# Performance work log

Measured on AMD Instinct MI355X. Metric: run time of the kernel, lower is better.

## Reference

```python
import math
import jax, jax.numpy as jnp
import numpy as np

T_LEN, BATCH = 215, 256
D_INP = 36; D_MODEL = 36          # d_model must be 36 for internal dims to be consistent
D_T = D_MODEL + 36                # 72: transformer encoder width
N_HEAD = 4; D_HEAD = D_T // N_HEAD
D_FF = 128; N_LAYERS = 2; D_STATIC = 9; N_CLASSES = 2
N_NODES = 36

def _layer_norm(x, g, b, eps=1e-5):
    mu = jnp.mean(x, -1, keepdims=True)
    var = jnp.mean((x - mu) ** 2, -1, keepdims=True)
    return (x - mu) / jnp.sqrt(var + eps) * g + b

def _forward(src, static, times, lengths, W_enc, b_enc, W_emb, b_emb, Wq, bq, Wk, bk, Wv, bv, Wskip, bskip, enc_in_w, enc_in_b, enc_out_w, enc_out_b, enc_ff1_w, enc_ff1_b, enc_ff2_w, enc_ff2_b, enc_ln1_g, enc_ln1_b, enc_ln2_g, enc_ln2_b, mlp_w1, mlp_b1, mlp_w2, mlp_b2):
    T, B = src.shape[0], src.shape[1]
    x = (src[:, :, :D_INP] @ W_enc.T + b_enc) * math.sqrt(D_MODEL)          # [T,B,36]
    # positional encoding: 18 timescales = max_len ** linspace(0,1,18)
    timescales = jnp.asarray(215.0 ** np.linspace(0.0, 1.0, D_MODEL // 2), jnp.float32)
    scaled = times[:, :, None] / timescales                                  # [T,B,18]
    pe = jnp.concatenate([jnp.sin(scaled), jnp.cos(scaled)], -1)             # [T,B,36]
    emb = static @ W_emb.T + b_emb                                           # [B,36]
    mask = jnp.arange(T)[None, :] >= lengths[:, None]                        # [B,T] True = pad
    # --- batched TransformerConv over fully-connected 36-node graph (replaces per-sample loop) ---
    q = x @ Wq.T + bq; k = x @ Wk.T + bk; v = x @ Wv.T + bv
    skip = x @ Wskip.T + bskip
    scores = jnp.einsum('ibe,jbe->bij', q[:N_NODES], k[:N_NODES]) / math.sqrt(36.0)  # i=tgt, j=src
    A = jax.nn.softmax(scores, -1)                      # per-target softmax over incoming edges
    msg = jnp.einsum('bij,jbe->ibe', A, v[:N_NODES])    # edge_weights are all ones
    gout = skip.at[:N_NODES].add(msg)                   # [T,B,36]; rows >= 36 have no in-edges
    # per-edge alpha flattened in nonzero(adj) order: e = src*36 + tgt
    alpha_all = A.transpose(0, 2, 1).reshape(B, N_NODES * N_NODES).T         # [1296,B]
    sq = jnp.sum(alpha_all ** 2, 0)
    d2 = jnp.maximum(sq[:, None] + sq[None, :] - 2.0 * (alpha_all.T @ alpha_all), 0.0)
    distance = jnp.mean(jnp.sqrt(jnp.where(d2 > 0, d2, 1.0)) * (d2 > 0))     # mean pairwise L2
    # --- 2-layer post-norm transformer encoder, width 72, key padding mask ---
    h = jnp.concatenate([gout, pe], -1)                                      # [T,B,72]
    neg = jnp.where(mask[:, None, None, :], -1e9, 0.0)                       # [B,1,1,T]
    for l in range(N_LAYERS):
        qkv = h @ enc_in_w[l].T + enc_in_b[l]
        qh, kh, vh = [t.reshape(T, B, N_HEAD, D_HEAD) for t in jnp.split(qkv, 3, -1)]
        s = jnp.einsum('tbhd,sbhd->bhts', qh, kh) / math.sqrt(D_HEAD) + neg
        ctx = jnp.einsum('bhts,sbhd->tbhd', jax.nn.softmax(s, -1), vh).reshape(T, B, D_T)
        h = _layer_norm(h + ctx @ enc_out_w[l].T + enc_out_b[l], enc_ln1_g[l], enc_ln1_b[l])
        ff = jax.nn.relu(h @ enc_ff1_w[l].T + enc_ff1_b[l]) @ enc_ff2_w[l].T + enc_ff2_b[l]
        h = _layer_norm(h + ff, enc_ln2_g[l], enc_ln2_b[l])
    # masked mean over time, denominator lengths+1 (as in original)
    valid = (~mask).astype(h.dtype).T[:, :, None]                            # [T,B,1]
    pooled = jnp.sum(h * valid, 0) / (lengths.astype(h.dtype)[:, None] + 1.0)
    feat = jnp.concatenate([pooled, emb], -1)                                # [B,108]
    logits = jax.nn.relu(feat @ mlp_w1.T + mlp_b1) @ mlp_w2.T + mlp_b2
    return logits, distance

def setup_inputs() -> dict:
    key = jax.random.key(0)
    ks = jax.random.split(key, 40)
    def nrm(i, shape, s=0.05):
        return jax.random.normal(ks[i], shape, jnp.float32) * s
    return {
        'src': jax.random.normal(ks[0], (T_LEN, BATCH, 2 * D_INP), jnp.float32),
        'static': jax.random.normal(ks[1], (BATCH, D_STATIC), jnp.float32),
        'times': jnp.tile(jnp.arange(T_LEN, dtype=jnp.float32)[:, None], (1, BATCH)),
        'lengths': jax.random.randint(ks[2], (BATCH,), 1, T_LEN + 1),
        'W_enc': nrm(3, (D_MODEL, D_INP)), 'b_enc': jnp.zeros((D_MODEL,), jnp.float32),
        'W_emb': nrm(4, (D_MODEL, D_STATIC)), 'b_emb': jnp.zeros((D_MODEL,), jnp.float32),
        'Wq': nrm(5, (36, 36)), 'bq': nrm(6, (36,)),
        'Wk': nrm(7, (36, 36)), 'bk': nrm(8, (36,)),
        'Wv': nrm(9, (36, 36)), 'bv': nrm(10, (36,)),
        'Wskip': nrm(11, (36, 36)), 'bskip': nrm(12, (36,)),
        'enc_in_w': nrm(13, (N_LAYERS, 3 * D_T, D_T)), 'enc_in_b': nrm(14, (N_LAYERS, 3 * D_T)),
        'enc_out_w': nrm(15, (N_LAYERS, D_T, D_T)), 'enc_out_b': nrm(16, (N_LAYERS, D_T)),
        'enc_ff1_w': nrm(17, (N_LAYERS, D_FF, D_T)), 'enc_ff1_b': nrm(18, (N_LAYERS, D_FF)),
        'enc_ff2_w': nrm(19, (N_LAYERS, D_T, D_FF)), 'enc_ff2_b': nrm(20, (N_LAYERS, D_T)),
        'enc_ln1_g': jnp.ones((N_LAYERS, D_T), jnp.float32), 'enc_ln1_b': jnp.zeros((N_LAYERS, D_T), jnp.float32),
        'enc_ln2_g': jnp.ones((N_LAYERS, D_T), jnp.float32), 'enc_ln2_b': jnp.zeros((N_LAYERS, D_T), jnp.float32),
        'mlp_w1': nrm(21, (108, 108)), 'mlp_b1': nrm(22, (108,)),
        'mlp_w2': nrm(23, (N_CLASSES, 108)), 'mlp_b2': nrm(24, (N_CLASSES,)),
    }

def reference(src, static, times, lengths, W_enc, b_enc, W_emb, b_emb, Wq, bq, Wk, bk, Wv, bv, Wskip, bskip, enc_in_w, enc_in_b, enc_out_w, enc_out_b, enc_ff1_w, enc_ff1_b, enc_ff2_w, enc_ff2_b, enc_ln1_g, enc_ln1_b, enc_ln2_g, enc_ln2_b, mlp_w1, mlp_b1, mlp_w2, mlp_b2):
    return _forward(src, static, times, lengths, W_enc, b_enc, W_emb, b_emb, Wq, bq, Wk, bk, Wv, bv, Wskip, bskip, enc_in_w, enc_in_b, enc_out_w, enc_out_b, enc_ff1_w, enc_ff1_b, enc_ff2_w, enc_ff2_b, enc_ln1_g, enc_ln1_b, enc_ln2_g, enc_ln2_b, mlp_w1, mlp_b1, mlp_w2, mlp_b2)
```

## Files before the change

### kernel.cpp

```cpp
#include <hip/hip_runtime.h>

#define TT 215
#define BB 256
#define ROWS (TT * BB)

typedef __attribute__((ext_vector_type(8))) short short8;
typedef __attribute__((ext_vector_type(4))) float f32x4;

__device__ __forceinline__ unsigned short f2bf_rn(float x) {
    unsigned int u = __float_as_uint(x);
    u = u + 0x7FFFu + ((u >> 16) & 1u);
    return (unsigned short)(u >> 16);
}
__device__ __forceinline__ float bf2f(unsigned short b) {
    return __uint_as_float(((unsigned int)b) << 16);
}

__global__ void k_prep(const float* __restrict__ enc_in_w, const float* __restrict__ ff1_w,
                       const float* __restrict__ ff2_w, const float* __restrict__ enc_out_w,
                       unsigned short* __restrict__ Whi, unsigned short* __restrict__ Wlo,
                       unsigned short* __restrict__ F1hi, unsigned short* __restrict__ F1lo,
                       unsigned short* __restrict__ F2hi, unsigned short* __restrict__ F2lo,
                       unsigned short* __restrict__ Ohi, unsigned short* __restrict__ Olo,
                       float* __restrict__ ts) {
    int g = blockIdx.x * 256 + threadIdx.x;
    if (g < 18) ts[g] = (float)pow(215.0, (double)g / 17.0);
    if (g < 2 * 216 * 96) {
        int l = g / (216 * 96), rem = g % (216 * 96);
        int o = rem / 96, k = rem % 96;
        float v = (k < 72) ? enc_in_w[((size_t)l * 216 + o) * 72 + k] : 0.f;
        unsigned short hi = f2bf_rn(v);
        Whi[g] = hi; Wlo[g] = f2bf_rn(v - bf2f(hi));
    }
    if (g < 2 * 128 * 96) {
        int l = g / (128 * 96), rem = g % (128 * 96);
        int j = rem / 96, k = rem % 96;
        float v = (k < 72) ? ff1_w[((size_t)l * 128 + j) * 72 + k] : 0.f;
        unsigned short hi = f2bf_rn(v);
        F1hi[g] = hi; F1lo[g] = f2bf_rn(v - bf2f(hi));
    }
    if (g < 2 * 72 * 128) {
        float v = ff2_w[g];
        unsigned short hi = f2bf_rn(v);
        F2hi[g] = hi; F2lo[g] = f2bf_rn(v - bf2f(hi));
    }
    if (g < 2 * 72 * 96) {
        int l = g / (72 * 96), rem = g % (72 * 96);
        int o = rem / 96, k = rem % 96;
        float v = (k < 72) ? enc_out_w[((size_t)l * 72 + o) * 72 + k] : 0.f;
        unsigned short hi = f2bf_rn(v);
        Ohi[g] = hi; Olo[g] = f2bf_rn(v - bf2f(hi));
    }
}

__global__ __launch_bounds__(256, 1) void k_enc1(const float* __restrict__ src,
                                                 const float* __restrict__ W,
                                                 const float* __restrict__ bias,
                                                 float* __restrict__ x) {
    int row = blockIdx.x * 256 + threadIdx.x;
    int o0 = blockIdx.y * 9;
    float s[36];
    const float4* sv = (const float4*)(src + (size_t)row * 72);
#pragma unroll
    for (int k = 0; k < 9; ++k) {
        float4 v = sv[k];
        s[4 * k] = v.x; s[4 * k + 1] = v.y; s[4 * k + 2] = v.z; s[4 * k + 3] = v.w;
    }
    float* xp = x + (size_t)row * 36 + o0;
#pragma unroll
    for (int o = 0; o < 9; ++o) {
        float a = bias[o0 + o];
        const float* w = W + (size_t)(o0 + o) * 36;
#pragma unroll
        for (int i = 0; i < 36; ++i) a = fmaf(s[i], w[i], a);
        xp[o] = a * 6.0f;
    }
}

__global__ __launch_bounds__(256, 1) void k_enc2(const float* __restrict__ x,
                                                 const float* __restrict__ W,
                                                 const float* __restrict__ bias,
                                                 float* __restrict__ h) {
    int row = blockIdx.x * 256 + threadIdx.x;
    int o0 = blockIdx.y * 9;
    float xr[36];
    const float4* xv = (const float4*)(x + (size_t)row * 36);
#pragma unroll
    for (int k = 0; k < 9; ++k) {
        float4 v = xv[k];
        xr[4 * k] = v.x; xr[4 * k + 1] = v.y; xr[4 * k + 2] = v.z; xr[4 * k + 3] = v.w;
    }
    float* hp = h + (size_t)row * 72 + o0;
#pragma unroll
    for (int o = 0; o < 9; ++o) {
        float a = bias[o0 + o];
        const float* w = W + (size_t)(o0 + o) * 36;
#pragma unroll
        for (int i = 0; i < 36; ++i) a = fmaf(xr[i], w[i], a);
        hp[o] = a;
    }
}

__global__ __launch_bounds__(256) void k_pe(const float* __restrict__ times,
                                            const float* __restrict__ ts,
                                            float* __restrict__ h) {
    int idx = blockIdx.x * 256 + threadIdx.x;
    int d = idx % 36, row = idx / 36;
    float t = times[row];
    float val;
    if (d < 18) val = sinf(t / ts[d]);
    else        val = cosf(t / ts[d - 18]);
    h[(size_t)row * 72 + 36 + d] = val;
}

__global__ __launch_bounds__(256, 1) void k_graph_qkv(const float* __restrict__ x,
                                                      const float* __restrict__ Wq, const float* __restrict__ bq,
                                                      const float* __restrict__ Wk, const float* __restrict__ bk,
                                                      const float* __restrict__ Wv, const float* __restrict__ bv,
                                                      float* __restrict__ qg, float* __restrict__ kg,
                                                      float* __restrict__ vg) {
    int row = blockIdx.x * 256 + threadIdx.x;
    int mat = blockIdx.y >> 2;
    int o0 = (blockIdx.y & 3) * 9;
    const float* W; const float* bias; float* out;
    if (mat == 0)      { W = Wq; bias = bq; out = qg; }
    else if (mat == 1) { W = Wk; bias = bk; out = kg; }
    else               { W = Wv; bias = bv; out = vg; }
    float xr[36];
    const float4* xv = (const float4*)(x + (size_t)row * 36);
#pragma unroll
    for (int k = 0; k < 9; ++k) {
        float4 v = xv[k];
        xr[4 * k] = v.x; xr[4 * k + 1] = v.y; xr[4 * k + 2] = v.z; xr[4 * k + 3] = v.w;
    }
    float* op = out + (size_t)row * 36 + o0;
#pragma unroll
    for (int o = 0; o < 9; ++o) {
        float a = bias[o0 + o];
        const float* w = W + (size_t)(o0 + o) * 36;
#pragma unroll
        for (int i = 0; i < 36; ++i) a = fmaf(xr[i], w[i], a);
        op[o] = a;
    }
}

__global__ void k_graph_attn(const float* __restrict__ qg, const float* __restrict__ kg,
                             const float* __restrict__ vg, float* __restrict__ h,
                             unsigned short* __restrict__ Ahi, unsigned short* __restrict__ Alo,
                             float* __restrict__ sqv) {
    __shared__ float q[1296], k[1296], v[1296], A[1296];
    __shared__ float red[128];
    int b = blockIdx.x, tid = threadIdx.x;
    for (int i = tid; i < 1296; i += 128) {
        int t = i / 36, e = i % 36;
        int g = (t * BB + b) * 36 + e;
        q[i] = qg[g]; k[i] = kg[g]; v[i] = vg[g];
    }
    __syncthreads();
    for (int i = tid; i < 1296; i += 128) {
        int r = i / 36, c = i % 36;
        float a = 0.f;
#pragma unroll
        for (int e = 0; e < 36; ++e) a = fmaf(q[r * 36 + e], k[c * 36 + e], a);
        A[i] = a * (1.0f / 6.0f);
    }
    __syncthreads();
    if (tid < 36) {
        float m = -1e30f;
        for (int j = 0; j < 36; ++j) m = fmaxf(m, A[tid * 36 + j]);
        float s = 0.f;
        for (int j = 0; j < 36; ++j) { float e = expf(A[tid * 36 + j] - m); A[tid * 36 + j] = e; s += e; }
        float inv = 1.0f / s;
        for (int j = 0; j < 36; ++j) A[tid * 36 + j] *= inv;
    }
    __syncthreads();
    float lsq = 0.f;
    for (int i = tid; i < 1296; i += 128) {
        float a = A[i];
        unsigned short hi = f2bf_rn(a);
        Ahi[(size_t)b * 1312 + i] = hi;
        Alo[(size_t)b * 1312 + i] = f2bf_rn(a - bf2f(hi));
        lsq = fmaf(a, a, lsq);
        int r = i / 36, e = i % 36;
        float m = 0.f;
#pragma unroll
        for (int j = 0; j < 36; ++j) m = fmaf(A[r * 36 + j], v[j * 36 + e], m);
        h[((size_t)r * BB + b) * 72 + e] += m;
    }
    if (tid < 16) {
        Ahi[(size_t)b * 1312 + 1296 + tid] = 0;
        Alo[(size_t)b * 1312 + 1296 + tid] = 0;
    }
    red[tid] = lsq;
    __syncthreads();
    for (int s = 64; s > 0; s >>= 1) { if (tid < s) red[tid] += red[tid + s]; __syncthreads(); }
    if (tid == 0) sqv[b] = red[0];
}

__global__ __launch_bounds__(256, 1) void k_gram(const unsigned short* __restrict__ Ahi,
                                                 const unsigned short* __restrict__ Alo,
                                                 const float* __restrict__ sqv,
                                                 float* __restrict__ bpart) {
    __shared__ float red[4];
    int tid = threadIdx.x;
    int w = tid >> 6;
    int lane = tid & 63;
    int n16 = lane & 15;
    int quad = lane >> 4;
    int i0 = (blockIdx.x >> 3) * 32 + (w >> 1) * 16;
    int j0 = (blockIdx.x & 7) * 32 + (w & 1) * 16;
    const short8* Ari = (const short8*)(Ahi + (size_t)(i0 + n16) * 1312);
    const short8* Arl = (const short8*)(Alo + (size_t)(i0 + n16) * 1312);
    const short8* Bri = (const short8*)(Ahi + (size_t)(j0 + n16) * 1312);
    const short8* Brl = (const short8*)(Alo + (size_t)(j0 + n16) * 1312);
    f32x4 acc = (f32x4){0.f, 0.f, 0.f, 0.f};
    for (int k2 = 0; k2 < 41; ++k2) {
        int ko = k2 * 4 + quad;
        short8 ah = Ari[ko], al = Arl[ko];
        short8 bh = Bri[ko], bl = Brl[ko];
        acc = __builtin_amdgcn_mfma_f32_16x16x32_bf16(ah, bh, acc, 0, 0, 0);
        acc = __builtin_amdgcn_mfma_f32_16x16x32_bf16(ah, bl, acc, 0, 0, 0);
        acc = __builtin_amdgcn_mfma_f32_16x16x32_bf16(al, bh, acc, 0, 0, 0);
    }
    float part = 0.f;
#pragma unroll
    for (int reg = 0; reg < 4; ++reg) {
        int i = i0 + quad * 4 + reg;
        int j = j0 + n16;
        float d2 = fmaxf(sqv[i] + sqv[j] - 2.0f * acc[reg], 0.0f);
        part += (d2 > 0.0f) ? sqrtf(d2) : 0.0f;
    }
#pragma unroll
    for (int m = 1; m < 64; m <<= 1) part += __shfl_xor(part, m);
    if (lane == 0) red[w] = part;
    __syncthreads();
    if (tid == 0) bpart[blockIdx.x] = red[0] + red[1] + red[2] + red[3];
}

__global__ __launch_bounds__(256, 1) void k_qkv(const float* __restrict__ h,
                                                const unsigned short* __restrict__ Whi,
                                                const unsigned short* __restrict__ Wlo,
                                                const float* __restrict__ bias,
                                                float* __restrict__ qkv) {
    int tid = threadIdx.x;
    int w = tid >> 6;
    int lane = tid & 63;
    int n16 = lane & 15;
    int quad = lane >> 4;
    int m0 = blockIdx.x * 64 + w * 16;
    int r = m0 + n16;
    short8 Ahi[3], Alo[3];
#pragma unroll
    for (int s = 0; s < 3; ++s) {
        int k0 = s * 32 + quad * 8;
        float v[8];
        if (k0 < 72) {
            const float4* ap = (const float4*)(h + (size_t)r * 72 + k0);
            float4 v0 = ap[0], v1 = ap[1];
            v[0] = v0.x; v[1] = v0.y; v[2] = v0.z; v[3] = v0.w;
            v[4] = v1.x; v[5] = v1.y; v[6] = v1.z; v[7] = v1.w;
        } else {
#pragma unroll
            for (int j = 0; j < 8; ++j) v[j] = 0.f;
        }
        short8 ph, pl;
#pragma unroll
        for (int j = 0; j < 8; ++j) {
            unsigned short hi = f2bf_rn(v[j]);
            ph[j] = (short)hi;
            pl[j] = (short)f2bf_rn(v[j] - bf2f(hi));
        }
        Ahi[s] = ph; Alo[s] = pl;
    }
    f32x4 acc[14];
#pragma unroll
    for (int t = 0; t < 14; ++t) acc[t] = (f32x4){0.f, 0.f, 0.f, 0.f};
#pragma unroll
    for (int t = 0; t < 14; ++t) {
        int o = t * 16 + n16;
        int oc = (o > 215) ? 215 : o;
        const short8* bh = (const short8*)(Whi + (size_t)oc * 96);
        const short8* bl = (const short8*)(Wlo + (size_t)oc * 96);
        f32x4 a = acc[t];
#pragma unroll
        for (int s = 0; s < 3; ++s) {
            short8 Bh = bh[s * 4 + quad];
            short8 Bl = bl[s * 4 + quad];
            a = __builtin_amdgcn_mfma_f32_16x16x32_bf16(Ahi[s], Bh, a, 0, 0, 0);
            a = __builtin_amdgcn_mfma_f32_16x16x32_bf16(Ahi[s], Bl, a, 0, 0, 0);
            a = __builtin_amdgcn_mfma_f32_16x16x32_bf16(Alo[s], Bh, a, 0, 0, 0);
        }
        acc[t] = a;
    }
#pragma unroll
    for (int t = 0; t < 14; ++t) {
        int col = t * 16 + n16;
        if (col < 216) {
            float b = bias[col];
#pragma unroll
            for (int reg = 0; reg < 4; ++reg) {
                int row = m0 + quad * 4 + reg;
                qkv[(size_t)row * 216 + col] = acc[t][reg] + b;
            }
        }
    }
}

__global__ __launch_bounds__(256, 1) void k_attn(const float* __restrict__ qkv,
                                                 const int* __restrict__ lengths,
                                                 float* __restrict__ ctx) {
    __shared__ __attribute__((aligned(16))) unsigned short Kb[215 * 40];
    __shared__ __attribute__((aligned(16))) unsigned short Vt[32 * 232];
    __shared__ __attribute__((aligned(16))) unsigned short Pw[4][16 * 232];
    int b = blockIdx.x & (BB - 1);
    int hh = blockIdx.x >> 8;
    int tid = threadIdx.x;
    int len = lengths[b];
    for (int i = tid; i < (215 * 40) / 2; i += 256) ((unsigned int*)Kb)[i] = 0u;
    for (int i = tid; i < (32 * 232) / 2; i += 256) ((unsigned int*)Vt)[i] = 0u;
    __syncthreads();
    for (int i = tid; i < len * 18; i += 256) {
        int s = i / 18, d = i % 18;
        size_t base2 = ((size_t)s * BB + b) * 216 + hh * 18 + d;
        Kb[s * 40 + d] = f2bf_rn(qkv[base2 + 72]);
        Vt[d * 232 + s] = f2bf_rn(qkv[base2 + 144]);
    }
    __syncthreads();
    int w = tid >> 6;
    int lane = tid & 63;
    int n16 = lane & 15;
    int quad = lane >> 4;
    const float scale = 0.23570226039551587f;
    int nk2 = (len + 31) >> 5;
    int nkt = nk2 * 2;
    int nstrips = (len + 15) >> 4;
    unsigned short* P = &Pw[w][0];
    for (int strip = w; strip < nstrips; strip += 4) {
        int q0 = strip * 16;
        int qr = q0 + n16; if (qr > 214) qr = 214;
        float qv[8];
#pragma unroll
        for (int j = 0; j < 8; ++j) qv[j] = 0.f;
        {
            const float* qp = qkv + ((size_t)qr * BB + b) * 216 + hh * 18;
            int d0 = quad * 8;
            if (d0 < 16) {
                const float2* q2 = (const float2*)(qp + d0);
                float2 a0 = q2[0], a1 = q2[1], a2 = q2[2], a3 = q2[3];
                qv[0] = a0.x; qv[1] = a0.y; qv[2] = a1.x; qv[3] = a1.y;
                qv[4] = a2.x; qv[5] = a2.y; qv[6] = a3.x; qv[7] = a3.y;
            } else if (d0 == 16) {
                qv[0] = qp[16]; qv[1] = qp[17];
            }
        }
        short8 Qhi, Qlo;
#pragma unroll
        for (int j = 0; j < 8; ++j) {
            float v = qv[j] * scale;
            unsigned short hi = f2bf_rn(v);
            Qhi[j] = (short)hi;
            Qlo[j] = (short)f2bf_rn(v - bf2f(hi));
        }
        float lsum[4] = {0.f, 0.f, 0.f, 0.f};
        for (int kt = 0; kt < nkt; ++kt) {
            int key = kt * 16 + n16;
            int kr = (key > 214) ? 214 : key;
            short8 Bk = *(const short8*)(Kb + kr * 40 + quad * 8);
            f32x4 S = (f32x4){0.f, 0.f, 0.f, 0.f};
            S = __builtin_amdgcn_mfma_f32_16x16x32_bf16(Qlo, Bk, S, 0, 0, 0);
            S = __builtin_amdgcn_mfma_f32_16x16x32_bf16(Qhi, Bk, S, 0, 0, 0);
#pragma unroll
            for (int reg = 0; reg < 4; ++reg) {
                float p = (key < len) ? __expf(S[reg]) : 0.f;
                lsum[reg] += p;
                P[(quad * 4 + reg) * 232 + kt * 16 + n16] = f2bf_rn(p);
            }
        }
#pragma unroll
        for (int m = 1; m < 16; m <<= 1) {
#pragma unroll
            for (int reg = 0; reg < 4; ++reg) lsum[reg] += __shfl_xor(lsum[reg], m);
        }
        f32x4 o0 = (f32x4){0.f, 0.f, 0.f, 0.f};
        f32x4 o1 = (f32x4){0.f, 0.f, 0.f, 0.f};
        for (int k2 = 0; k2 < nk2; ++k2) {
            short8 Af = *(const short8*)(P + n16 * 232 + k2 * 32 + quad * 8);
            short8 Bv0 = *(const short8*)(Vt + n16 * 232 + k2 * 32 + quad * 8);
            short8 Bv1 = *(const short8*)(Vt + (16 + n16) * 232 + k2 * 32 + quad * 8);
            o0 = __builtin_amdgcn_mfma_f32_16x16x32_bf16(Af, Bv0, o0, 0, 0, 0);
            o1 = __builtin_amdgcn_mfma_f32_16x16x32_bf16(Af, Bv1, o1, 0, 0, 0);
        }
#pragma unroll
        for (int reg = 0; reg < 4; ++reg) {
            int t = q0 + quad * 4 + reg;
            if (t < len) {
                float inv = 1.0f / lsum[reg];
                float* cb = ctx + ((size_t)t * BB + b) * 72 + hh * 18;
                cb[n16] = o0[reg] * inv;
                if (n16 < 2) cb[16 + n16] = o1[reg] * inv;
            }
        }
    }
}

__global__ __launch_bounds__(256, 1) void k_outln(const float* __restrict__ ctx,
                                                  const unsigned short* __restrict__ Ohi,
                                                  const unsigned short* __restrict__ Olo,
                                                  const float* __restrict__ bias,
                                                  const float* __restrict__ g,
                                                  const float* __restrict__ beta,
                                                  float* __restrict__ h) {
    int tid = threadIdx.x;
    int w = tid >> 6;
    int lane = tid & 63;
    int n16 = lane & 15;
    int quad = lane >> 4;
    int m0 = blockIdx.x * 64 + w * 16;
    int r = m0 + n16;
    short8 Ahi[3], Alo[3];
#pragma unroll
    for (int s = 0; s < 3; ++s) {
        int k0 = s * 32 + quad * 8;
        float v[8];
        if (k0 < 72) {
            const float4* ap = (const float4*)(ctx + (size_t)r * 72 + k0);
            float4 v0 = ap[0], v1 = ap[1];
            v[0] = v0.x; v[1] = v0.y; v[2] = v0.z; v[3] = v0.w;
            v[4] = v1.x; v[5] = v1.y; v[6] = v1.z; v[7] = v1.w;
        } else {
#pragma unroll
            for (int j = 0; j < 8; ++j) v[j] = 0.f;
        }
        short8 ph, pl;
#pragma unroll
        for (int j = 0; j < 8; ++j) {
            unsigned short hi = f2bf_rn(v[j]);
            ph[j] = (short)hi;
            pl[j] = (short)f2bf_rn(v[j] - bf2f(hi));
        }
        Ahi[s] = ph; Alo[s] = pl;
    }
    f32x4 acc[5];
#pragma unroll
    for (int t = 0; t < 5; ++t) acc[t] = (f32x4){0.f, 0.f, 0.f, 0.f};
#pragma unroll
    for (int t = 0; t < 5; ++t) {
        int o = t * 16 + n16;
        int oc = (o > 71) ? 71 : o;
        const short8* bh = (const short8*)(Ohi + (size_t)oc * 96);
        const short8* bl = (const short8*)(Olo + (size_t)oc * 96);
        f32x4 a = acc[t];
#pragma unroll
        for (int s = 0; s < 3; ++s) {
            short8 Bh = bh[s * 4 + quad];
            short8 Bl = bl[s * 4 + quad];
            a = __builtin_amdgcn_mfma_f32_16x16x32_bf16(Ahi[s], Bh, a, 0, 0, 0);
            a = __builtin_amdgcn_mfma_f32_16x16x32_bf16(Ahi[s], Bl, a, 0, 0, 0);
            a = __builtin_amdgcn_mfma_f32_16x16x32_bf16(Alo[s], Bh, a, 0, 0, 0);
        }
        acc[t] = a;
    }
    float vals[5][4];
#pragma unroll
    for (int t = 0; t < 5; ++t) {
        int o = t * 16 + n16;
        bool valid = (o < 72);
        float bb = valid ? bias[o] : 0.f;
#pragma unroll
        for (int reg = 0; reg < 4; ++reg) {
            int row = m0 + quad * 4 + reg;
            float hv = valid ? h[(size_t)row * 72 + o] : 0.f;
            vals[t][reg] = acc[t][reg] + bb + hv;
        }
    }
#pragma unroll
    for (int reg = 0; reg < 4; ++reg) {
        float s = 0.f, q = 0.f;
#pragma unroll
        for (int t = 0; t < 5; ++t) {
            int o = t * 16 + n16;
            if (o < 72) { s += vals[t][reg]; q = fmaf(vals[t][reg], vals[t][reg], q); }
        }
#pragma unroll
        for (int m = 1; m < 16; m <<= 1) { s += __shfl_xor(s, m); q += __shfl_xor(q, m); }
        float mu = s / 72.0f;
        float var = fmaxf(q / 72.0f - mu * mu, 0.0f);
        float rstd = 1.0f / sqrtf(var + 1e-5f);
        int row = m0 + quad * 4 + reg;
#pragma unroll
        for (int t = 0; t < 5; ++t) {
            int o = t * 16 + n16;
            if (o < 72)
                h[(size_t)row * 72 + o] = (vals[t][reg] - mu) * rstd * g[o] + beta[o];
        }
    }
}

__global__ __launch_bounds__(256, 1) void k_ffln(const unsigned short* __restrict__ F1hi,
                                                 const unsigned short* __restrict__ F1lo,
                                                 const float* __restrict__ b1,
                                                 const unsigned short* __restrict__ F2hi,
                                                 const unsigned short* __restrict__ F2lo,
                                                 const float* __restrict__ b2,
                                                 const float* __restrict__ g,
                                                 const float* __restrict__ beta,
                                                 float* __restrict__ h) {
    __shared__ float hid[64][129];
    int tid = threadIdx.x;
    int w = tid >> 6;
    int lane = tid & 63;
    int n16 = lane & 15;
    int quad = lane >> 4;
    int m0 = blockIdx.x * 64 + w * 16;
    int r = m0 + n16;
    short8 Ahi[3], Alo[3];
#pragma unroll
    for (int s = 0; s < 3; ++s) {
        int k0 = s * 32 + quad * 8;
        float v[8];
        if (k0 < 72) {
            const float4* ap = (const float4*)(h + (size_t)r * 72 + k0);
            float4 v0 = ap[0], v1 = ap[1];
            v[0] = v0.x; v[1] = v0.y; v[2] = v0.z; v[3] = v0.w;
            v[4] = v1.x; v[5] = v1.y; v[6] = v1.z; v[7] = v1.w;
        } else {
#pragma unroll
            for (int j = 0; j < 8; ++j) v[j] = 0.f;
        }
        short8 ph, pl;
#pragma unroll
        for (int j = 0; j < 8; ++j) {
            unsigned short hi = f2bf_rn(v[j]);
            ph[j] = (short)hi;
            pl[j] = (short)f2bf_rn(v[j] - bf2f(hi));
        }
        Ahi[s] = ph; Alo[s] = pl;
    }
#pragma unroll
    for (int t = 0; t < 8; ++t) {
        int j = t * 16 + n16;
        const short8* bh = (const short8*)(F1hi + (size_t)j * 96);
        const short8* bl = (const short8*)(F1lo + (size_t)j * 96);
        f32x4 a = (f32x4){0.f, 0.f, 0.f, 0.f};
#pragma unroll
        for (int s = 0; s < 3; ++s) {
            short8 Bh = bh[s * 4 + quad];
            short8 Bl = bl[s * 4 + quad];
            a = __builtin_amdgcn_mfma_f32_16x16x32_bf16(Ahi[s], Bh, a, 0, 0, 0);
            a = __builtin_amdgcn_mfma_f32_16x16x32_bf16(Ahi[s], Bl, a, 0, 0, 0);
            a = __builtin_amdgcn_mfma_f32_16x16x32_bf16(Alo[s], Bh, a, 0, 0, 0);
        }
        float bb = b1[j];
#pragma unroll
        for (int reg = 0; reg < 4; ++reg)
            hid[w * 16 + quad * 4 + reg][j] = fmaxf(a[reg] + bb, 0.f);
    }
    short8 A2hi[4], A2lo[4];
#pragma unroll
    for (int s = 0; s < 4; ++s) {
        const float* hp = &hid[w * 16 + n16][s * 32 + quad * 8];
        short8 ph, pl;
#pragma unroll
        for (int j = 0; j < 8; ++j) {
            float v = hp[j];
            unsigned short hi = f2bf_rn(v);
            ph[j] = (short)hi;
            pl[j] = (short)f2bf_rn(v - bf2f(hi));
        }
        A2hi[s] = ph; A2lo[s] = pl;
    }
    f32x4 acc[5];
#pragma unroll
    for (int t = 0; t < 5; ++t) acc[t] = (f32x4){0.f, 0.f, 0.f, 0.f};
#pragma unroll
    for (int t = 0; t < 5; ++t) {
        int o = t * 16 + n16;
        int oc = (o > 71) ? 71 : o;
        const short8* bh = (const short8*)(F2hi + (size_t)oc * 128);
        const short8* bl = (const short8*)(F2lo + (size_t)oc * 128);
        f32x4 a = acc[t];
#pragma unroll
        for (int s = 0; s < 4; ++s) {
            short8 Bh = bh[s * 4 + quad];
            short8 Bl = bl[s * 4 + quad];
            a = __builtin_amdgcn_mfma_f32_16x16x32_bf16(A2hi[s], Bh, a, 0, 0, 0);
            a = __builtin_amdgcn_mfma_f32_16x16x32_bf16(A2hi[s], Bl, a, 0, 0, 0);
            a = __builtin_amdgcn_mfma_f32_16x16x32_bf16(A2lo[s], Bh, a, 0, 0, 0);
        }
        acc[t] = a;
    }
    float vals[5][4];
#pragma unroll
    for (int t = 0; t < 5; ++t) {
        int o = t * 16 + n16;
        bool valid = (o < 72);
        float bb = valid ? b2[o] : 0.f;
#pragma unroll
        for (int reg = 0; reg < 4; ++reg) {
            int row = m0 + quad * 4 + reg;
            float hv = valid ? h[(size_t)row * 72 + o] : 0.f;
            vals[t][reg] = acc[t][reg] + bb + hv;
        }
    }
#pragma unroll
    for (int reg = 0; reg < 4; ++reg) {
        float s = 0.f, q = 0.f;
#pragma unroll
        for (int t = 0; t < 5; ++t) {
            int o = t * 16 + n16;
            if (o < 72) { s += vals[t][reg]; q = fmaf(vals[t][reg], vals[t][reg], q); }
        }
#pragma unroll
        for (int m = 1; m < 16; m <<= 1) { s += __shfl_xor(s, m); q += __shfl_xor(q, m); }
        float mu = s / 72.0f;
        float var = fmaxf(q / 72.0f - mu * mu, 0.0f);
        float rstd = 1.0f / sqrtf(var + 1e-5f);
        int row = m0 + quad * 4 + reg;
#pragma unroll
        for (int t = 0; t < 5; ++t) {
            int o = t * 16 + n16;
            if (o < 72)
                h[(size_t)row * 72 + o] = (vals[t][reg] - mu) * rstd * g[o] + beta[o];
        }
    }
}

__global__ void k_head(const float* __restrict__ h, const int* __restrict__ lengths,
                       const float* __restrict__ statics, const float* __restrict__ W_emb,
                       const float* __restrict__ b_emb, const float* __restrict__ w1,
                       const float* __restrict__ bb1, const float* __restrict__ w2,
                       const float* __restrict__ bb2, float* __restrict__ out) {
    __shared__ float ps2[4][72];
    __shared__ float feat[108];
    __shared__ float hidm[108];
    __shared__ float st[9];
    int b = blockIdx.x, tid = threadIdx.x;
    int w = tid >> 6, lane = tid & 63;
    int len = lengths[b];
    if (tid < 9) st[tid] = statics[b * 9 + tid];
    for (int idx = tid; idx < 288; idx += 256) ((float*)ps2)[idx] = 0.f;
    __syncthreads();
#pragma unroll
    for (int c0 = 0; c0 < 128; c0 += 64) {
        int col = c0 + lane;
        if (col < 72) {
            float s = 0.f;
            for (int t = w; t < len; t += 4) s += h[((size_t)t * BB + b) * 72 + col];
            ps2[w][col] = s;
        }
    }
    __syncthreads();
    if (tid < 72)
        feat[tid] = (ps2[0][tid] + ps2[1][tid] + ps2[2][tid] + ps2[3][tid]) / ((float)len + 1.0f);
    if (tid >= 128 && tid < 164) {
        int o = tid - 128;
        float a = b_emb[o];
#pragma unroll
        for (int i = 0; i < 9; ++i) a = fmaf(st[i], W_emb[o * 9 + i], a);
        feat[72 + o] = a;
    }
    __syncthreads();
    if (tid < 108) {
        float a = bb1[tid];
        for (int i = 0; i < 108; ++i) a = fmaf(feat[i], w1[tid * 108 + i], a);
        hidm[tid] = fmaxf(a, 0.f);
    }
    __syncthreads();
    if (tid < 2) {
        float a = bb2[tid];
        for (int i = 0; i < 108; ++i) a = fmaf(hidm[i], w2[tid * 108 + i], a);
        out[b * 2 + tid] = a;
    }
}

__global__ void k_dist(const float* __restrict__ bpart, float* __restrict__ out) {
    __shared__ float red[64];
    int tid = threadIdx.x;
    red[tid] = bpart[tid];
    __syncthreads();
    for (int s = 32; s > 0; s >>= 1) { if (tid < s) red[tid] += red[tid + s]; __syncthreads(); }
    if (tid == 0) out[2 * BB] = red[0] / 65536.0f;
}

extern "C" void kernel_launch(void* const* d_in, const int* in_sizes, int n_in,
                              void* d_out, int out_size, void* d_ws, size_t ws_size,
                              hipStream_t stream) {
    const float* src     = (const float*)d_in[0];
    const float* statics = (const float*)d_in[1];
    const float* times   = (const float*)d_in[2];
    const int*   lengths = (const int*)d_in[3];
    const float* W_enc = (const float*)d_in[4];  const float* b_enc = (const float*)d_in[5];
    const float* W_emb = (const float*)d_in[6];  const float* b_emb = (const float*)d_in[7];
    const float* Wq = (const float*)d_in[8];     const float* bq = (const float*)d_in[9];
    const float* Wk = (const float*)d_in[10];    const float* bk = (const float*)d_in[11];
    const float* Wv = (const float*)d_in[12];    const float* bv = (const float*)d_in[13];
    const float* Wskip = (const float*)d_in[14]; const float* bskip = (const float*)d_in[15];
    const float* enc_in_w = (const float*)d_in[16];  const float* enc_in_b = (const float*)d_in[17];
    const float* enc_out_w = (const float*)d_in[18]; const float* enc_out_b = (const float*)d_in[19];
    const float* ff1_w = (const float*)d_in[20]; const float* ff1_b = (const float*)d_in[21];
    const float* ff2_w = (const float*)d_in[22]; const float* ff2_b = (const float*)d_in[23];
    const float* ln1_g = (const float*)d_in[24]; const float* ln1_b = (const float*)d_in[25];
    const float* ln2_g = (const float*)d_in[26]; const float* ln2_b = (const float*)d_in[27];
    const float* w1 = (const float*)d_in[28];    const float* bb1 = (const float*)d_in[29];
    const float* w2 = (const float*)d_in[30];    const float* bb2 = (const float*)d_in[31];
    float* out = (float*)d_out;

    float* p = (float*)d_ws;
    float* x    = p; p += (size_t)ROWS * 36;
    float* h    = p; p += (size_t)ROWS * 72;
    float* qkv  = p; p += (size_t)ROWS * 216;
    float* ctx  = p; p += (size_t)ROWS * 72;
    float* qg   = p; p += (size_t)36 * BB * 36;
    float* kg   = p; p += (size_t)36 * BB * 36;
    float* vg   = p; p += (size_t)36 * BB * 36;
    float* sqv  = p; p += BB;
    float* bpart = p; p += 64;
    float* ts   = p; p += 32;
    unsigned short* GAhi = (unsigned short*)p; p += (BB * 1312) / 2;
    unsigned short* GAlo = (unsigned short*)p; p += (BB * 1312) / 2;
    unsigned short* Whi  = (unsigned short*)p; p += (2 * 216 * 96) / 2;
    unsigned short* Wlo  = (unsigned short*)p; p += (2 * 216 * 96) / 2;
    unsigned short* F1hi = (unsigned short*)p; p += (2 * 128 * 96) / 2;
    unsigned short* F1lo = (unsigned short*)p; p += (2 * 128 * 96) / 2;
    unsigned short* F2hi = (unsigned short*)p; p += (2 * 72 * 128) / 2;
    unsigned short* F2lo = (unsigned short*)p; p += (2 * 72 * 128) / 2;
    unsigned short* Ohi  = (unsigned short*)p; p += (2 * 72 * 96) / 2;
    unsigned short* Olo  = (unsigned short*)p; p += (2 * 72 * 96) / 2;

    k_prep<<<162, 256, 0, stream>>>(enc_in_w, ff1_w, ff2_w, enc_out_w,
                                    Whi, Wlo, F1hi, F1lo, F2hi, F2lo, Ohi, Olo, ts);
    k_enc1<<<dim3(TT, 4), 256, 0, stream>>>(src, W_enc, b_enc, x);
    k_enc2<<<dim3(TT, 4), 256, 0, stream>>>(x, Wskip, bskip, h);
    k_pe<<<(ROWS * 36) / 256, 256, 0, stream>>>(times, ts, h);
    k_graph_qkv<<<dim3(36, 12), 256, 0, stream>>>(x, Wq, bq, Wk, bk, Wv, bv, qg, kg, vg);
    k_graph_attn<<<BB, 128, 0, stream>>>(qg, kg, vg, h, GAhi, GAlo, sqv);
    k_gram<<<64, 256, 0, stream>>>(GAhi, GAlo, sqv, bpart);
    for (int l = 0; l < 2; ++l) {
        k_qkv<<<ROWS / 64, 256, 0, stream>>>(h, Whi + (size_t)l * 216 * 96,
                                             Wlo + (size_t)l * 216 * 96,
                                             enc_in_b + l * 216, qkv);
        k_attn<<<BB * 4, 256, 0, stream>>>(qkv, lengths, ctx);
        k_outln<<<ROWS / 64, 256, 0, stream>>>(ctx, Ohi + (size_t)l * 72 * 96,
                                               Olo + (size_t)l * 72 * 96, enc_out_b + l * 72,
                                               ln1_g + l * 72, ln1_b + l * 72, h);
        k_ffln<<<ROWS / 64, 256, 0, stream>>>(F1hi + (size_t)l * 128 * 96,
                                              F1lo + (size_t)l * 128 * 96, ff1_b + l * 128,
                                              F2hi + (size_t)l * 72 * 128,
                                              F2lo + (size_t)l * 72 * 128, ff2_b + l * 72,
                                              ln2_g + l * 72, ln2_b + l * 72, h);
    }
    k_head<<<BB, 256, 0, stream>>>(h, lengths, statics, W_emb, b_emb, w1, bb1, w2, bb2, out);
    k_dist<<<1, 64, 0, stream>>>(bpart, out);
}
```

Before: 474.0 us.

## Fuse encoder projections with positional encoding and interleave attention softmax with PV

k_enc1 and k_enc2 now compute all 36 outputs per thread instead of splitting the outputs across four grid columns, so each input row is read once. The positional-encoding kernel is folded into k_enc2pe, which removes one launch. In k_attn, probabilities are now written to a small 32-key LDS tile and consumed right away by the PV MFMA per chunk. The full 232-wide P buffer is gone, which cuts LDS footprint and traffic. The trade-off is a 36-accumulator register load per thread and a smaller grid for the encoder kernels.

```diff
diff --git a/kernel.cpp b/kernel.cpp
--- a/kernel.cpp
+++ b/kernel.cpp
@@ -58,7 +58,6 @@
                                                  const float* __restrict__ bias,
                                                  float* __restrict__ x) {
     int row = blockIdx.x * 256 + threadIdx.x;
-    int o0 = blockIdx.y * 9;
     float s[36];
     const float4* sv = (const float4*)(src + (size_t)row * 72);
 #pragma unroll
@@ -66,23 +65,28 @@
         float4 v = sv[k];
         s[4 * k] = v.x; s[4 * k + 1] = v.y; s[4 * k + 2] = v.z; s[4 * k + 3] = v.w;
     }
-    float* xp = x + (size_t)row * 36 + o0;
-#pragma unroll
-    for (int o = 0; o < 9; ++o) {
-        float a = bias[o0 + o];
-        const float* w = W + (size_t)(o0 + o) * 36;
-#pragma unroll
-        for (int i = 0; i < 36; ++i) a = fmaf(s[i], w[i], a);
-        xp[o] = a * 6.0f;
-    }
-}
-
-__global__ __launch_bounds__(256, 1) void k_enc2(const float* __restrict__ x,
-                                                 const float* __restrict__ W,
-                                                 const float* __restrict__ bias,
-                                                 float* __restrict__ h) {
+    float acc[36];
+#pragma unroll
+    for (int o = 0; o < 36; ++o) acc[o] = bias[o];
+#pragma unroll
+    for (int i = 0; i < 36; ++i) {
+#pragma unroll
+        for (int o = 0; o < 36; ++o) acc[o] = fmaf(s[i], W[o * 36 + i], acc[o]);
+    }
+    float4* xv = (float4*)(x + (size_t)row * 36);
+#pragma unroll
+    for (int k = 0; k < 9; ++k)
+        xv[k] = make_float4(acc[4 * k] * 6.f, acc[4 * k + 1] * 6.f,
+                            acc[4 * k + 2] * 6.f, acc[4 * k + 3] * 6.f);
+}
+
+__global__ __launch_bounds__(256, 1) void k_enc2pe(const float* __restrict__ x,
+                                                   const float* __restrict__ times,
+                                                   const float* __restrict__ W,
+                                                   const float* __restrict__ bias,
+                                                   const float* __restrict__ ts,
+                                                   float* __restrict__ h) {
     int row = blockIdx.x * 256 + threadIdx.x;
-    int o0 = blockIdx.y * 9;
     float xr[36];
     const float4* xv = (const float4*)(x + (size_t)row * 36);
 #pragma unroll
@@ -90,27 +94,26 @@
         float4 v = xv[k];
         xr[4 * k] = v.x; xr[4 * k + 1] = v.y; xr[4 * k + 2] = v.z; xr[4 * k + 3] = v.w;
     }
-    float* hp = h + (size_t)row * 72 + o0;
-#pragma unroll
-    for (int o = 0; o < 9; ++o) {
-        float a = bias[o0 + o];
-        const float* w = W + (size_t)(o0 + o) * 36;
-#pragma unroll
-        for (int i = 0; i < 36; ++i) a = fmaf(xr[i], w[i], a);
-        hp[o] = a;
-    }
-}
-
-__global__ __launch_bounds__(256) void k_pe(const float* __restrict__ times,
-                                            const float* __restrict__ ts,
-                                            float* __restrict__ h) {
-    int idx = blockIdx.x * 256 + threadIdx.x;
-    int d = idx % 36, row = idx / 36;
+    float acc[36];
+#pragma unroll
+    for (int o = 0; o < 36; ++o) acc[o] = bias[o];
+#pragma unroll
+    for (int i = 0; i < 36; ++i) {
+#pragma unroll
+        for (int o = 0; o < 36; ++o) acc[o] = fmaf(xr[i], W[o * 36 + i], acc[o]);
+    }
+    float* hr = h + (size_t)row * 72;
+    float4* hv = (float4*)hr;
+#pragma unroll
+    for (int k = 0; k < 9; ++k)
+        hv[k] = make_float4(acc[4 * k], acc[4 * k + 1], acc[4 * k + 2], acc[4 * k + 3]);
     float t = times[row];
-    float val;
-    if (d < 18) val = sinf(t / ts[d]);
-    else        val = cosf(t / ts[d - 18]);
-    h[(size_t)row * 72 + 36 + d] = val;
+#pragma unroll
+    for (int d = 0; d < 18; ++d) {
+        float sc = t / ts[d];
+        hr[36 + d] = sinf(sc);
+        hr[54 + d] = cosf(sc);
+    }
 }
 
 __global__ __launch_bounds__(256, 1) void k_graph_qkv(const float* __restrict__ x,
@@ -311,7 +314,7 @@
                                                  float* __restrict__ ctx) {
     __shared__ __attribute__((aligned(16))) unsigned short Kb[215 * 40];
     __shared__ __attribute__((aligned(16))) unsigned short Vt[32 * 232];
-    __shared__ __attribute__((aligned(16))) unsigned short Pw[4][16 * 232];
+    __shared__ __attribute__((aligned(16))) unsigned short Pw[4][16 * 40];
     int b = blockIdx.x & (BB - 1);
     int hh = blockIdx.x >> 8;
     int tid = threadIdx.x;
@@ -332,7 +335,6 @@
     int quad = lane >> 4;
     const float scale = 0.23570226039551587f;
     int nk2 = (len + 31) >> 5;
-    int nkt = nk2 * 2;
     int nstrips = (len + 15) >> 4;
     unsigned short* P = &Pw[w][0];
     for (int strip = w; strip < nstrips; strip += 4) {
@@ -362,33 +364,34 @@
             Qlo[j] = (short)f2bf_rn(v - bf2f(hi));
         }
         float lsum[4] = {0.f, 0.f, 0.f, 0.f};
-        for (int kt = 0; kt < nkt; ++kt) {
-            int key = kt * 16 + n16;
-            int kr = (key > 214) ? 214 : key;
-            short8 Bk = *(const short8*)(Kb + kr * 40 + quad * 8);
-            f32x4 S = (f32x4){0.f, 0.f, 0.f, 0.f};
-            S = __builtin_amdgcn_mfma_f32_16x16x32_bf16(Qlo, Bk, S, 0, 0, 0);
-            S = __builtin_amdgcn_mfma_f32_16x16x32_bf16(Qhi, Bk, S, 0, 0, 0);
-#pragma unroll
-            for (int reg = 0; reg < 4; ++reg) {
-                float p = (key < len) ? __expf(S[reg]) : 0.f;
-                lsum[reg] += p;
-                P[(quad * 4 + reg) * 232 + kt * 16 + n16] = f2bf_rn(p);
-            }
-        }
-#pragma unroll
-        for (int m = 1; m < 16; m <<= 1) {
-#pragma unroll
-            for (int reg = 0; reg < 4; ++reg) lsum[reg] += __shfl_xor(lsum[reg], m);
-        }
         f32x4 o0 = (f32x4){0.f, 0.f, 0.f, 0.f};
         f32x4 o1 = (f32x4){0.f, 0.f, 0.f, 0.f};
-        for (int k2 = 0; k2 < nk2; ++k2) {
-            short8 Af = *(const short8*)(P + n16 * 232 + k2 * 32 + quad * 8);
-            short8 Bv0 = *(const short8*)(Vt + n16 * 232 + k2 * 32 + quad * 8);
-            short8 Bv1 = *(const short8*)(Vt + (16 + n16) * 232 + k2 * 32 + quad * 8);
+        for (int kc = 0; kc < nk2; ++kc) {
+#pragma unroll
+            for (int t2 = 0; t2 < 2; ++t2) {
+                int key = kc * 32 + t2 * 16 + n16;
+                int kr = (key > 214) ? 214 : key;
+                short8 Bk = *(const short8*)(Kb + kr * 40 + quad * 8);
+                f32x4 S = (f32x4){0.f, 0.f, 0.f, 0.f};
+                S = __builtin_amdgcn_mfma_f32_16x16x32_bf16(Qlo, Bk, S, 0, 0, 0);
+                S = __builtin_amdgcn_mfma_f32_16x16x32_bf16(Qhi, Bk, S, 0, 0, 0);
+#pragma unroll
+                for (int reg = 0; reg < 4; ++reg) {
+                    float p = (key < len) ? __expf(S[reg]) : 0.f;
+                    lsum[reg] += p;
+                    P[(quad * 4 + reg) * 40 + t2 * 16 + n16] = f2bf_rn(p);
+                }
+            }
+            short8 Af = *(const short8*)(P + n16 * 40 + quad * 8);
+            short8 Bv0 = *(const short8*)(Vt + n16 * 232 + kc * 32 + quad * 8);
+            short8 Bv1 = *(const short8*)(Vt + (16 + n16) * 232 + kc * 32 + quad * 8);
             o0 = __builtin_amdgcn_mfma_f32_16x16x32_bf16(Af, Bv0, o0, 0, 0, 0);
             o1 = __builtin_amdgcn_mfma_f32_16x16x32_bf16(Af, Bv1, o1, 0, 0, 0);
+        }
+#pragma unroll
+        for (int m = 1; m < 16; m <<= 1) {
+#pragma unroll
+            for (int reg = 0; reg < 4; ++reg) lsum[reg] += __shfl_xor(lsum[reg], m);
         }
 #pragma unroll
         for (int reg = 0; reg < 4; ++reg) {
@@ -729,9 +732,8 @@
 
     k_prep<<<162, 256, 0, stream>>>(enc_in_w, ff1_w, ff2_w, enc_out_w,
                                     Whi, Wlo, F1hi, F1lo, F2hi, F2lo, Ohi, Olo, ts);
-    k_enc1<<<dim3(TT, 4), 256, 0, stream>>>(src, W_enc, b_enc, x);
-    k_enc2<<<dim3(TT, 4), 256, 0, stream>>>(x, Wskip, bskip, h);
-    k_pe<<<(ROWS * 36) / 256, 256, 0, stream>>>(times, ts, h);
+    k_enc1<<<TT, 256, 0, stream>>>(src, W_enc, b_enc, x);
+    k_enc2pe<<<TT, 256, 0, stream>>>(x, times, Wskip, bskip, ts, h);
     k_graph_qkv<<<dim3(36, 12), 256, 0, stream>>>(x, Wq, bq, Wk, bk, Wv, bv, qg, kg, vg);
     k_graph_attn<<<BB, 128, 0, stream>>>(qg, kg, vg, h, GAhi, GAlo, sqv);
     k_gram<<<64, 256, 0, stream>>>(GAhi, GAlo, sqv, bpart);
```

After: 478.5 us. Within noise of the previous version (+1.0%).
